# Performance work log

Measured on AMD Instinct MI355X. Metric: run time of the kernel, lower is better.

Reference implementation:

```python
import math
import jax, jax.numpy as jnp
import numpy as np

B, H, S, D = 2, 16, 2048, 64

def setup_inputs() -> dict:
    key = jax.random.key(0)
    kq, kk, kv, km = jax.random.split(key, 4)
    q = jax.random.normal(kq, (B, H, S, D), dtype=jnp.float32)
    k = jax.random.normal(kk, (B, H, S, D), dtype=jnp.float32)
    v = jax.random.normal(kv, (B, H, S, D), dtype=jnp.float32)
    mask = jax.random.randint(km, (B, S, S), 0, 2, dtype=jnp.int32)
    return {"q": q, "k": k, "v": v, "mask": mask}

def reference(q, k, v, mask):
    # attn = q @ (k^T / sqrt(d))  -> [B,H,Sq,Sk]
    scale = 1.0 / math.sqrt(q.shape[-1])
    attn = jnp.einsum("bhqd,bhkd->bhqk", q, k * scale)
    # masked_fill where mask.unsqueeze(1) == 1
    attn = jnp.where(mask[:, None, :, :] == 1, jnp.float32(-1e9), attn)
    attn = jax.nn.softmax(attn, axis=-1)
    # dropout is identity in eval / p=0
    res = jnp.einsum("bhqk,bhkd->bhqd", attn, v)
    return (res, attn)
```

## Files before the change

kernel.cpp:

```cpp
#include <hip/hip_runtime.h>

#define B_ 2
#define H_ 16
#define S_ 2048
#define D_ 64
#define QB 32
#define KT 64
#define NTHREADS 512

typedef _Float16 f16;
typedef _Float16 f16x8 __attribute__((ext_vector_type(8)));
typedef _Float16 f16x4 __attribute__((ext_vector_type(4)));
typedef _Float16 f16x2 __attribute__((ext_vector_type(2)));
typedef float f32x4 __attribute__((ext_vector_type(4)));

#define MFMA16(a, b, c) __builtin_amdgcn_mfma_f32_16x16x32_f16(a, b, c, 0, 0, 0)

__global__ __launch_bounds__(NTHREADS)
void attn_kernel(const float* __restrict__ q, const float* __restrict__ k,
                 const float* __restrict__ v, const int* __restrict__ mask,
                 float* __restrict__ out)
{
    __shared__ f16 Qsh[QB][D_ + 8];
    __shared__ f16 Ksh[KT][D_ + 8];
    __shared__ f16 Vsh[KT][D_ + 2];
    __shared__ f16 Psh[QB][KT + 8];
    __shared__ float rowred[QB];
    __shared__ float rlsh[QB];

    const int tid  = threadIdx.x;
    const int wave = tid >> 6;
    const int lane = tid & 63;
    const int quad = lane >> 4;
    const int l16  = lane & 15;
    const int qi   = wave & 1;
    const int ni   = wave >> 1;

    const int qb = blockIdx.x;
    const int h  = blockIdx.y;
    const int b  = blockIdx.z;
    const int bh = b * H_ + h;

    const float* Qg = q + ((size_t)bh * S_ + (size_t)qb * QB) * D_;
    const float* Kg = k + (size_t)bh * S_ * D_;
    const float* Vg = v + (size_t)bh * S_ * D_;
    const int*   Mg = mask + ((size_t)b * S_ + (size_t)qb * QB) * S_;
    float* res_out  = out + ((size_t)bh * S_ + (size_t)qb * QB) * D_;
    float* attn_out = out + (size_t)B_ * H_ * S_ * D_
                          + ((size_t)bh * S_ + (size_t)qb * QB) * S_;

    if (tid < QB) rowred[tid] = 0.f;

    {
        const int row = tid >> 4;
        const int c4  = (tid & 15) * 4;
        const float4 qv = *(const float4*)(Qg + row * D_ + c4);
        f16x4 o;
        o[0] = (f16)(qv.x * 0.125f); o[1] = (f16)(qv.y * 0.125f);
        o[2] = (f16)(qv.z * 0.125f); o[3] = (f16)(qv.w * 0.125f);
        *(f16x4*)&Qsh[row][c4] = o;
    }
    __syncthreads();

    const int qrow0 = qi * 16 + quad * 4;
    const f16x8 a0 = *(const f16x8*)&Qsh[qi * 16 + l16][quad * 8];
    const f16x8 a1 = *(const f16x8*)&Qsh[qi * 16 + l16][32 + quad * 8];

    const int colbase = ni * 16 + l16;
    const int* mp0 = Mg + (size_t)qrow0 * S_ + colbase;

    const int skk = tid >> 3;
    const int sd0 = (tid & 7) * 8;

    float psum[4] = {0.f, 0.f, 0.f, 0.f};
    for (int kt = 0; kt < S_ / KT; ++kt) {
        {
            const float* src = Kg + ((size_t)(kt * KT + skk)) * D_ + sd0;
            const float4 x0 = *(const float4*)(src);
            const float4 x1 = *(const float4*)(src + 4);
            f16x8 o;
            o[0] = (f16)x0.x; o[1] = (f16)x0.y; o[2] = (f16)x0.z; o[3] = (f16)x0.w;
            o[4] = (f16)x1.x; o[5] = (f16)x1.y; o[6] = (f16)x1.z; o[7] = (f16)x1.w;
            *(f16x8*)&Ksh[skk][sd0] = o;
        }
        __syncthreads();
        const f16x8 b0 = *(const f16x8*)&Ksh[ni * 16 + l16][quad * 8];
        const f16x8 b1 = *(const f16x8*)&Ksh[ni * 16 + l16][32 + quad * 8];
        f32x4 c = {0.f, 0.f, 0.f, 0.f};
        c = MFMA16(a0, b0, c);
        c = MFMA16(a1, b1, c);
        const int* mp = mp0 + kt * KT;
#pragma unroll
        for (int r = 0; r < 4; ++r) {
            const int m = mp[(size_t)r * S_];
            const float e = (m == 1) ? 0.f : __expf(c[r]);
            psum[r] += e;
        }
        __syncthreads();
    }

#pragma unroll
    for (int r = 0; r < 4; ++r) {
        psum[r] += __shfl_xor(psum[r], 1);
        psum[r] += __shfl_xor(psum[r], 2);
        psum[r] += __shfl_xor(psum[r], 4);
        psum[r] += __shfl_xor(psum[r], 8);
    }
    if (l16 == 0) {
#pragma unroll
        for (int r = 0; r < 4; ++r) atomicAdd(&rowred[qrow0 + r], psum[r]);
    }
    __syncthreads();
    if (tid < QB) rlsh[tid] = 1.0f / rowred[tid];
    __syncthreads();
    float rlq[4];
#pragma unroll
    for (int r = 0; r < 4; ++r) rlq[r] = rlsh[qrow0 + r];

    f32x4 oacc = {0.f, 0.f, 0.f, 0.f};
    float* ap0 = attn_out + (size_t)qrow0 * S_ + colbase;

    for (int kt = 0; kt < S_ / KT; ++kt) {
        {
            const float* srck = Kg + ((size_t)(kt * KT + skk)) * D_ + sd0;
            const float4 x0 = *(const float4*)(srck);
            const float4 x1 = *(const float4*)(srck + 4);
            f16x8 o;
            o[0] = (f16)x0.x; o[1] = (f16)x0.y; o[2] = (f16)x0.z; o[3] = (f16)x0.w;
            o[4] = (f16)x1.x; o[5] = (f16)x1.y; o[6] = (f16)x1.z; o[7] = (f16)x1.w;
            *(f16x8*)&Ksh[skk][sd0] = o;

            const float* srcv = Vg + ((size_t)(kt * KT + skk)) * D_ + sd0;
            const float4 y0 = *(const float4*)(srcv);
            const float4 y1 = *(const float4*)(srcv + 4);
            f16x2 p01, p23, p45, p67;
            p01[0] = (f16)y0.x; p01[1] = (f16)y0.y;
            p23[0] = (f16)y0.z; p23[1] = (f16)y0.w;
            p45[0] = (f16)y1.x; p45[1] = (f16)y1.y;
            p67[0] = (f16)y1.z; p67[1] = (f16)y1.w;
            *(f16x2*)&Vsh[skk][sd0]     = p01;
            *(f16x2*)&Vsh[skk][sd0 + 2] = p23;
            *(f16x2*)&Vsh[skk][sd0 + 4] = p45;
            *(f16x2*)&Vsh[skk][sd0 + 6] = p67;
        }
        __syncthreads();
        const f16x8 b0 = *(const f16x8*)&Ksh[ni * 16 + l16][quad * 8];
        const f16x8 b1 = *(const f16x8*)&Ksh[ni * 16 + l16][32 + quad * 8];
        f32x4 c = {0.f, 0.f, 0.f, 0.f};
        c = MFMA16(a0, b0, c);
        c = MFMA16(a1, b1, c);
        const int* mp = mp0 + kt * KT;
        float* ap = ap0 + kt * KT;
#pragma unroll
        for (int r = 0; r < 4; ++r) {
            const int m = mp[(size_t)r * S_];
            const float e = (m == 1) ? 0.f : __expf(c[r]);
            const float p = e * rlq[r];
            ap[(size_t)r * S_] = p;
            Psh[qrow0 + r][colbase] = (f16)p;
        }
        __syncthreads();
        const f16x8 pa0 = *(const f16x8*)&Psh[qi * 16 + l16][quad * 8];
        const f16x8 pa1 = *(const f16x8*)&Psh[qi * 16 + l16][32 + quad * 8];
        f16x8 vb0, vb1;
        const int dcol = ni * 16 + l16;
#pragma unroll
        for (int j = 0; j < 8; ++j) {
            vb0[j] = Vsh[quad * 8 + j][dcol];
            vb1[j] = Vsh[32 + quad * 8 + j][dcol];
        }
        oacc = MFMA16(pa0, vb0, oacc);
        oacc = MFMA16(pa1, vb1, oacc);
        __syncthreads();
    }

#pragma unroll
    for (int r = 0; r < 4; ++r)
        res_out[(size_t)(qrow0 + r) * D_ + ni * 16 + l16] = oacc[r];
}

extern "C" void kernel_launch(void* const* d_in, const int* in_sizes, int n_in,
                              void* d_out, int out_size, void* d_ws, size_t ws_size,
                              hipStream_t stream) {
    (void)in_sizes; (void)n_in; (void)out_size; (void)d_ws; (void)ws_size;
    const float* q   = (const float*)d_in[0];
    const float* k   = (const float*)d_in[1];
    const float* v   = (const float*)d_in[2];
    const int*  mask = (const int*)d_in[3];
    float* out = (float*)d_out;
    dim3 grid(S_ / QB, H_, B_);
    attn_kernel<<<grid, dim3(NTHREADS), 0, stream>>>(q, k, v, mask, out);
}
```

Baseline: 836.2 us.

## Fuse two-pass softmax into a single pass with register-cached exps and prefetching

Merges the row-sum pass and the P·V pass into one loop. Unnormalised exponentials are kept in registers (as f16) and fed to the PV MFMA, with the output scaled by the reciprocal row sum at the end, so K, the mask and the exp no longer have to be recomputed in a second pass. Loads of the next K/V/mask tile are software-prefetched into double/triple-buffered shared memory, leaving one barrier per iteration. In exchange, the 32-entry f16x4 register cache adds heavy register pressure, which may cause spills or lower occupancy. The attn output is now rounded to f16 before normalisation, which costs precision.

Measured after the change: 901.3 us. +7.8%, slower.

```diff
diff --git a/kernel.cpp b/kernel.cpp
--- a/kernel.cpp
+++ b/kernel.cpp
@@ -6,7 +6,8 @@
 #define D_ 64
 #define QB 32
 #define KT 64
-#define NTHREADS 512
+#define NKT (S_ / KT)
+#define NT 512
 
 typedef _Float16 f16;
 typedef _Float16 f16x8 __attribute__((ext_vector_type(8)));
@@ -16,15 +17,20 @@
 
 #define MFMA16(a, b, c) __builtin_amdgcn_mfma_f32_16x16x32_f16(a, b, c, 0, 0, 0)
 
-__global__ __launch_bounds__(NTHREADS)
+#define KS 72
+#define VS 66
+#define PS 72
+#define QS 72
+
+__global__ __launch_bounds__(NT, 4)
 void attn_kernel(const float* __restrict__ q, const float* __restrict__ k,
                  const float* __restrict__ v, const int* __restrict__ mask,
                  float* __restrict__ out)
 {
-    __shared__ f16 Qsh[QB][D_ + 8];
-    __shared__ f16 Ksh[KT][D_ + 8];
-    __shared__ f16 Vsh[KT][D_ + 2];
-    __shared__ f16 Psh[QB][KT + 8];
+    __shared__ __align__(16) f16 Qsh[QB][QS];
+    __shared__ __align__(16) f16 Ksh[2][KT][KS];
+    __shared__ __align__(16) f16 Vsh[3][KT][VS];
+    __shared__ __align__(16) f16 Psh[2][QB][PS];
     __shared__ float rowred[QB];
     __shared__ float rlsh[QB];
 
@@ -50,6 +56,9 @@
                           + ((size_t)bh * S_ + (size_t)qb * QB) * S_;
 
     if (tid < QB) rowred[tid] = 0.f;
+
+    const int skk = tid >> 3;
+    const int sd0 = (tid & 7) * 8;
 
     {
         const int row = tid >> 4;
@@ -60,6 +69,26 @@
         o[2] = (f16)(qv.z * 0.125f); o[3] = (f16)(qv.w * 0.125f);
         *(f16x4*)&Qsh[row][c4] = o;
     }
+
+    {
+        const float* sk = Kg + (size_t)skk * D_ + sd0;
+        const float4 x0 = *(const float4*)sk, x1 = *(const float4*)(sk + 4);
+        const float* sv = Vg + (size_t)skk * D_ + sd0;
+        const float4 y0 = *(const float4*)sv, y1 = *(const float4*)(sv + 4);
+        f16x8 ko;
+        ko[0] = (f16)x0.x; ko[1] = (f16)x0.y; ko[2] = (f16)x0.z; ko[3] = (f16)x0.w;
+        ko[4] = (f16)x1.x; ko[5] = (f16)x1.y; ko[6] = (f16)x1.z; ko[7] = (f16)x1.w;
+        *(f16x8*)&Ksh[0][skk][sd0] = ko;
+        f16x2 p0, p1, p2, p3;
+        p0[0] = (f16)y0.x; p0[1] = (f16)y0.y;
+        p1[0] = (f16)y0.z; p1[1] = (f16)y0.w;
+        p2[0] = (f16)y1.x; p2[1] = (f16)y1.y;
+        p3[0] = (f16)y1.z; p3[1] = (f16)y1.w;
+        *(f16x2*)&Vsh[0][skk][sd0]     = p0;
+        *(f16x2*)&Vsh[0][skk][sd0 + 2] = p1;
+        *(f16x2*)&Vsh[0][skk][sd0 + 4] = p2;
+        *(f16x2*)&Vsh[0][skk][sd0 + 6] = p3;
+    }
     __syncthreads();
 
     const int qrow0 = qi * 16 + quad * 4;
@@ -69,34 +98,79 @@
     const int colbase = ni * 16 + l16;
     const int* mp0 = Mg + (size_t)qrow0 * S_ + colbase;
 
-    const int skk = tid >> 3;
-    const int sd0 = (tid & 7) * 8;
+    int mcur[4];
+#pragma unroll
+    for (int r = 0; r < 4; ++r) mcur[r] = mp0[(size_t)r * S_];
 
     float psum[4] = {0.f, 0.f, 0.f, 0.f};
-    for (int kt = 0; kt < S_ / KT; ++kt) {
-        {
-            const float* src = Kg + ((size_t)(kt * KT + skk)) * D_ + sd0;
-            const float4 x0 = *(const float4*)(src);
-            const float4 x1 = *(const float4*)(src + 4);
-            f16x8 o;
-            o[0] = (f16)x0.x; o[1] = (f16)x0.y; o[2] = (f16)x0.z; o[3] = (f16)x0.w;
-            o[4] = (f16)x1.x; o[5] = (f16)x1.y; o[6] = (f16)x1.z; o[7] = (f16)x1.w;
-            *(f16x8*)&Ksh[skk][sd0] = o;
-        }
-        __syncthreads();
-        const f16x8 b0 = *(const f16x8*)&Ksh[ni * 16 + l16][quad * 8];
-        const f16x8 b1 = *(const f16x8*)&Ksh[ni * 16 + l16][32 + quad * 8];
+    f32x4 oacc = {0.f, 0.f, 0.f, 0.f};
+    f16x4 ereg[NKT];
+
+#pragma unroll
+    for (int kt = 0; kt < NKT; ++kt) {
+        const int cur  = kt & 1, nxt = cur ^ 1;
+        const int vcur = kt % 3, vnxt = (kt + 1) % 3;
+
+        float4 kx0, kx1, vx0, vx1;
+        int mn[4];
+        if (kt < NKT - 1) {
+            const float* sk = Kg + (size_t)((kt + 1) * KT + skk) * D_ + sd0;
+            kx0 = *(const float4*)sk; kx1 = *(const float4*)(sk + 4);
+            const float* sv = Vg + (size_t)((kt + 1) * KT + skk) * D_ + sd0;
+            vx0 = *(const float4*)sv; vx1 = *(const float4*)(sv + 4);
+            const int* mp = mp0 + (kt + 1) * KT;
+#pragma unroll
+            for (int r = 0; r < 4; ++r) mn[r] = mp[(size_t)r * S_];
+        }
+
+        const f16x8 b0 = *(const f16x8*)&Ksh[cur][ni * 16 + l16][quad * 8];
+        const f16x8 b1 = *(const f16x8*)&Ksh[cur][ni * 16 + l16][32 + quad * 8];
         f32x4 c = {0.f, 0.f, 0.f, 0.f};
         c = MFMA16(a0, b0, c);
         c = MFMA16(a1, b1, c);
-        const int* mp = mp0 + kt * KT;
+
+        f16x4 ev;
 #pragma unroll
         for (int r = 0; r < 4; ++r) {
-            const int m = mp[(size_t)r * S_];
-            const float e = (m == 1) ? 0.f : __expf(c[r]);
+            const float e = (mcur[r] == 1) ? 0.f : __expf(c[r]);
             psum[r] += e;
-        }
+            ev[r] = (f16)e;
+        }
+        ereg[kt] = ev;
+#pragma unroll
+        for (int r = 0; r < 4; ++r) Psh[cur][qrow0 + r][colbase] = ev[r];
+
+        if (kt < NKT - 1) {
+            f16x8 ko;
+            ko[0] = (f16)kx0.x; ko[1] = (f16)kx0.y; ko[2] = (f16)kx0.z; ko[3] = (f16)kx0.w;
+            ko[4] = (f16)kx1.x; ko[5] = (f16)kx1.y; ko[6] = (f16)kx1.z; ko[7] = (f16)kx1.w;
+            *(f16x8*)&Ksh[nxt][skk][sd0] = ko;
+            f16x2 p0, p1, p2, p3;
+            p0[0] = (f16)vx0.x; p0[1] = (f16)vx0.y;
+            p1[0] = (f16)vx0.z; p1[1] = (f16)vx0.w;
+            p2[0] = (f16)vx1.x; p2[1] = (f16)vx1.y;
+            p3[0] = (f16)vx1.z; p3[1] = (f16)vx1.w;
+            *(f16x2*)&Vsh[vnxt][skk][sd0]     = p0;
+            *(f16x2*)&Vsh[vnxt][skk][sd0 + 2] = p1;
+            *(f16x2*)&Vsh[vnxt][skk][sd0 + 4] = p2;
+            *(f16x2*)&Vsh[vnxt][skk][sd0 + 6] = p3;
+#pragma unroll
+            for (int r = 0; r < 4; ++r) mcur[r] = mn[r];
+        }
+
         __syncthreads();
+
+        const f16x8 pa0 = *(const f16x8*)&Psh[cur][qi * 16 + l16][quad * 8];
+        const f16x8 pa1 = *(const f16x8*)&Psh[cur][qi * 16 + l16][32 + quad * 8];
+        f16x8 vb0, vb1;
+        const int dcol = ni * 16 + l16;
+#pragma unroll
+        for (int j = 0; j < 8; ++j) {
+            vb0[j] = Vsh[vcur][quad * 8 + j][dcol];
+            vb1[j] = Vsh[vcur][32 + quad * 8 + j][dcol];
+        }
+        oacc = MFMA16(pa0, vb0, oacc);
+        oacc = MFMA16(pa1, vb1, oacc);
     }
 
 #pragma unroll
@@ -117,66 +191,17 @@
 #pragma unroll
     for (int r = 0; r < 4; ++r) rlq[r] = rlsh[qrow0 + r];
 
-    f32x4 oacc = {0.f, 0.f, 0.f, 0.f};
     float* ap0 = attn_out + (size_t)qrow0 * S_ + colbase;
-
-    for (int kt = 0; kt < S_ / KT; ++kt) {
-        {
-            const float* srck = Kg + ((size_t)(kt * KT + skk)) * D_ + sd0;
-            const float4 x0 = *(const float4*)(srck);
-            const float4 x1 = *(const float4*)(srck + 4);
-            f16x8 o;
-            o[0] = (f16)x0.x; o[1] = (f16)x0.y; o[2] = (f16)x0.z; o[3] = (f16)x0.w;
-            o[4] = (f16)x1.x; o[5] = (f16)x1.y; o[6] = (f16)x1.z; o[7] = (f16)x1.w;
-            *(f16x8*)&Ksh[skk][sd0] = o;
-
-            const float* srcv = Vg + ((size_t)(kt * KT + skk)) * D_ + sd0;
-            const float4 y0 = *(const float4*)(srcv);
-            const float4 y1 = *(const float4*)(srcv + 4);
-            f16x2 p01, p23, p45, p67;
-            p01[0] = (f16)y0.x; p01[1] = (f16)y0.y;
-            p23[0] = (f16)y0.z; p23[1] = (f16)y0.w;
-            p45[0] = (f16)y1.x; p45[1] = (f16)y1.y;
-            p67[0] = (f16)y1.z; p67[1] = (f16)y1.w;
-            *(f16x2*)&Vsh[skk][sd0]     = p01;
-            *(f16x2*)&Vsh[skk][sd0 + 2] = p23;
-            *(f16x2*)&Vsh[skk][sd0 + 4] = p45;
-            *(f16x2*)&Vsh[skk][sd0 + 6] = p67;
-        }
-        __syncthreads();
-        const f16x8 b0 = *(const f16x8*)&Ksh[ni * 16 + l16][quad * 8];
-        const f16x8 b1 = *(const f16x8*)&Ksh[ni * 16 + l16][32 + quad * 8];
-        f32x4 c = {0.f, 0.f, 0.f, 0.f};
-        c = MFMA16(a0, b0, c);
-        c = MFMA16(a1, b1, c);
-        const int* mp = mp0 + kt * KT;
-        float* ap = ap0 + kt * KT;
-#pragma unroll
-        for (int r = 0; r < 4; ++r) {
-            const int m = mp[(size_t)r * S_];
-            const float e = (m == 1) ? 0.f : __expf(c[r]);
-            const float p = e * rlq[r];
-            ap[(size_t)r * S_] = p;
-            Psh[qrow0 + r][colbase] = (f16)p;
-        }
-        __syncthreads();
-        const f16x8 pa0 = *(const f16x8*)&Psh[qi * 16 + l16][quad * 8];
-        const f16x8 pa1 = *(const f16x8*)&Psh[qi * 16 + l16][32 + quad * 8];
-        f16x8 vb0, vb1;
-        const int dcol = ni * 16 + l16;
-#pragma unroll
-        for (int j = 0; j < 8; ++j) {
-            vb0[j] = Vsh[quad * 8 + j][dcol];
-            vb1[j] = Vsh[32 + quad * 8 + j][dcol];
-        }
-        oacc = MFMA16(pa0, vb0, oacc);
-        oacc = MFMA16(pa1, vb1, oacc);
-        __syncthreads();
+#pragma unroll
+    for (int kt = 0; kt < NKT; ++kt) {
+#pragma unroll
+        for (int r = 0; r < 4; ++r)
+            ap0[(size_t)r * S_ + kt * KT] = (float)ereg[kt][r] * rlq[r];
     }
 
 #pragma unroll
     for (int r = 0; r < 4; ++r)
-        res_out[(size_t)(qrow0 + r) * D_ + ni * 16 + l16] = oacc[r];
+        res_out[(size_t)(qrow0 + r) * D_ + ni * 16 + l16] = oacc[r] * rlq[r];
 }
 
 extern "C" void kernel_launch(void* const* d_in, const int* in_sizes, int n_in,
@@ -189,5 +214,5 @@
     const int*  mask = (const int*)d_in[3];
     float* out = (float*)d_out;
     dim3 grid(S_ / QB, H_, B_);
-    attn_kernel<<<grid, dim3(NTHREADS), 0, stream>>>(q, k, v, mask, out);
+    attn_kernel<<<grid, dim3(NT), 0, stream>>>(q, k, v, mask, out);
 }
```
